# Performance work log

Hardware: AMD Instinct MI355X
Metric: run time of the kernel (lower is better)

The kernel has to match this reference:

```python
import jax, jax.numpy as jnp
import numpy as np

RADIUS = 0.1
MAX_GRID_DIM = 96
MAX_COLLISIONS = 128
INCLUDE_SELF = True


def setup_inputs() -> dict:
    key = jax.random.key(0)
    k1, k2, k3 = jax.random.split(key, 3)
    B, N, M, D, C = 2, 8192, 8192, 3, 64
    locs = jax.random.uniform(k1, (B, N, D), dtype=jnp.float32)
    data = jax.random.normal(k2, (B, N, C), dtype=jnp.float32)
    qlocs = jax.random.uniform(k3, (B, M, D), dtype=jnp.float32)
    return {"locs": locs, "data": data, "qlocs": qlocs}


def _hashgrid_order(locs):
    """Returns idxs [B,N] int32 sorting particles by flattened hash-grid cell id.
       idxs[b,i] = original index of the particle at new position i."""
    lower = jnp.min(locs, axis=1, keepdims=True)          # [B,1,D]
    upper = jnp.max(locs, axis=1, keepdims=True)          # [B,1,D]
    # grid dims per batch/dim, cell width = radius, capped at max_grid_dim
    gd = jnp.clip(jnp.floor((upper - lower) / RADIUS).astype(jnp.int32) + 1,
                  1, MAX_GRID_DIM)                        # [B,1,D]
    cell = jnp.floor((locs - lower) / RADIUS).astype(jnp.int32)
    cell = jnp.clip(cell, 0, gd - 1)                      # [B,N,D]
    # mixed-radix flatten: stride[d] = prod(gd[d+1:])
    strides = jnp.concatenate(
        [jnp.cumprod(gd[..., ::-1], axis=-1)[..., ::-1][..., 1:],
         jnp.ones_like(gd[..., :1])], axis=-1)            # [B,1,D]
    cid = jnp.sum(cell * strides, axis=-1)                # [B,N]
    return jnp.argsort(cid, axis=1, stable=True).astype(jnp.int32)


def _collisions(qlocs, nlocs):
    """For each query, indices into reordered locs within RADIUS, lowest-index
       first, padded with -1 up to MAX_COLLISIONS. Returns [B,M,K] int32."""
    B, N, _ = nlocs.shape
    d2 = jnp.sum((qlocs[:, :, None, :] - nlocs[:, None, :, :]) ** 2, axis=-1)  # [B,M,N]
    mask = d2 <= RADIUS * RADIUS
    if not INCLUDE_SELF:
        mask = mask & (d2 > 0)
    # key = particle index if neighbor else N (sentinel); first K after sort
    key = jnp.where(mask, jnp.arange(N, dtype=jnp.int32)[None, None, :], N)
    first_k = jnp.sort(key, axis=-1)[..., :MAX_COLLISIONS]                     # [B,M,K]
    return jnp.where(first_k < N, first_k, -1).astype(jnp.int32)


def reference(locs, data, qlocs):
    idxs = _hashgrid_order(locs)                              # [B,N]
    nlocs = jnp.take_along_axis(locs, idxs[..., None], axis=1)   # reordered locs
    ndata = jnp.take_along_axis(data, idxs[..., None], axis=1)   # reordered data
    neighbors = _collisions(qlocs, nlocs)                     # [B,M,K]
    return nlocs, ndata, idxs, neighbors
```

## Files before the change

kernel.cpp:

```cpp
#include <hip/hip_runtime.h>
#include <cfloat>
#include <math.h>

#define BB 2
#define NN 8192
#define MM 8192
#define CC 64
#define RAD 0.1f
#define R2 0.01f
#define MAXK 128
#define CELL_CAP 4096
#define CS_STRIDE 4100

#define WS_HDR 0
#define WS_SIDX 32
#define WS_CS (WS_SIDX + BB*NN)
#define WS_NL4 (WS_CS + BB*CS_STRIDE)

__device__ __forceinline__ int cell_of(float v, float lo, int g) {
    int c = (int)floorf(__fdiv_rn(v - lo, RAD));
    return min(max(c, 0), g - 1);
}

__global__ __launch_bounds__(1024) void build_kernel(const float* __restrict__ locs,
                                                     int* __restrict__ ws,
                                                     float* __restrict__ idxs_out) {
    const int b = blockIdx.x;
    const int t = threadIdx.x;
    const int lane = t & 63;
    const int wid = t >> 6;
    __shared__ int s_start[CELL_CAP + 1];
    __shared__ int s_aux[16];
    __shared__ int s_tmp[NN];
    __shared__ int s_cid[NN];
    __shared__ float s_red6[16 * 6];
    __shared__ float s_lo[3];
    __shared__ int   s_g[3];
    __shared__ int   s_str[2];

    const float* L = locs + (size_t)b * NN * 3;

    float mn0 = FLT_MAX, mn1 = FLT_MAX, mn2 = FLT_MAX;
    float mx0 = -FLT_MAX, mx1 = -FLT_MAX, mx2 = -FLT_MAX;
    for (int i = t; i < NN; i += 1024) {
        float x = L[i*3+0], y = L[i*3+1], z = L[i*3+2];
        mn0 = fminf(mn0, x); mx0 = fmaxf(mx0, x);
        mn1 = fminf(mn1, y); mx1 = fmaxf(mx1, y);
        mn2 = fminf(mn2, z); mx2 = fmaxf(mx2, z);
    }
    #pragma unroll
    for (int d = 1; d < 64; d <<= 1) {
        mn0 = fminf(mn0, __shfl_xor(mn0, d, 64));
        mn1 = fminf(mn1, __shfl_xor(mn1, d, 64));
        mn2 = fminf(mn2, __shfl_xor(mn2, d, 64));
        mx0 = fmaxf(mx0, __shfl_xor(mx0, d, 64));
        mx1 = fmaxf(mx1, __shfl_xor(mx1, d, 64));
        mx2 = fmaxf(mx2, __shfl_xor(mx2, d, 64));
    }
    if (lane == 0) {
        s_red6[wid*6+0] = mn0; s_red6[wid*6+1] = mn1; s_red6[wid*6+2] = mn2;
        s_red6[wid*6+3] = mx0; s_red6[wid*6+4] = mx1; s_red6[wid*6+5] = mx2;
    }
    for (int c = t; c < CELL_CAP + 1; c += 1024) s_start[c] = 0;
    __syncthreads();
    if (t == 0) {
        float lo0 = FLT_MAX, lo1 = FLT_MAX, lo2 = FLT_MAX;
        float up0 = -FLT_MAX, up1 = -FLT_MAX, up2 = -FLT_MAX;
        for (int w = 0; w < 16; ++w) {
            lo0 = fminf(lo0, s_red6[w*6+0]); lo1 = fminf(lo1, s_red6[w*6+1]);
            lo2 = fminf(lo2, s_red6[w*6+2]);
            up0 = fmaxf(up0, s_red6[w*6+3]); up1 = fmaxf(up1, s_red6[w*6+4]);
            up2 = fmaxf(up2, s_red6[w*6+5]);
        }
        int g0 = min(max((int)floorf(__fdiv_rn(up0 - lo0, RAD)) + 1, 1), 96);
        int g1 = min(max((int)floorf(__fdiv_rn(up1 - lo1, RAD)) + 1, 1), 96);
        int g2 = min(max((int)floorf(__fdiv_rn(up2 - lo2, RAD)) + 1, 1), 96);
        s_lo[0] = lo0; s_lo[1] = lo1; s_lo[2] = lo2;
        s_g[0] = g0; s_g[1] = g1; s_g[2] = g2;
        s_str[0] = g1 * g2; s_str[1] = g2;
        int* hdr = ws + WS_HDR + b * 16;
        hdr[0] = __float_as_int(lo0); hdr[1] = __float_as_int(lo1); hdr[2] = __float_as_int(lo2);
        hdr[3] = g0; hdr[4] = g1; hdr[5] = g2;
        hdr[6] = g1 * g2; hdr[7] = g2; hdr[8] = g0 * g1 * g2;
    }
    __syncthreads();
    const float lo0 = s_lo[0], lo1 = s_lo[1], lo2f = s_lo[2];
    const int g0 = s_g[0], g1 = s_g[1], g2 = s_g[2];
    const int st0 = s_str[0], st1 = s_str[1];
    const int ncells = g0 * g1 * g2;

    for (int i = t; i < NN; i += 1024) {
        int c0 = cell_of(L[i*3+0], lo0, g0);
        int c1 = cell_of(L[i*3+1], lo1, g1);
        int c2 = cell_of(L[i*3+2], lo2f, g2);
        int cid = c0*st0 + c1*st1 + c2;
        s_cid[i] = cid;
        atomicAdd(&s_start[cid], 1);
    }
    __syncthreads();

    int base4 = t * 4;
    int v0 = s_start[base4], v1 = s_start[base4+1], v2 = s_start[base4+2], v3 = s_start[base4+3];
    int sum = v0 + v1 + v2 + v3;
    int x = sum;
    #pragma unroll
    for (int d = 1; d < 64; d <<= 1) {
        int v = __shfl_up(x, d, 64);
        if (lane >= d) x += v;
    }
    if (lane == 63) s_aux[wid] = x;
    __syncthreads();
    if (wid == 0) {
        int w = (lane < 16) ? s_aux[lane] : 0;
        #pragma unroll
        for (int d = 1; d < 16; d <<= 1) {
            int v = __shfl_up(w, d, 64);
            if (lane >= d) w += v;
        }
        if (lane < 16) s_aux[lane] = w;
    }
    __syncthreads();
    int waveoff = (wid == 0) ? 0 : s_aux[wid - 1];
    int run = waveoff + x - sum;
    s_start[base4]   = run;
    s_start[base4+1] = run + v0;
    s_start[base4+2] = run + v0 + v1;
    s_start[base4+3] = run + v0 + v1 + v2;
    if (t == 1023) s_start[CELL_CAP] = run + sum;
    __syncthreads();

    for (int i = t; i < NN; i += 1024) {
        int pos = atomicAdd(&s_start[s_cid[i]], 1);
        s_tmp[pos] = i;
    }
    __syncthreads();

    int* cs = ws + WS_CS + b * CS_STRIDE;
    for (int c = t; c <= ncells; c += 1024) cs[c] = (c == 0) ? 0 : s_start[c - 1];

    int* sIdx = ws + WS_SIDX + b * NN;
    for (int p = t; p < NN; p += 1024) {
        int i = s_tmp[p];
        int cid = s_cid[i];
        int segs = (cid == 0) ? 0 : s_start[cid - 1];
        int sege = s_start[cid];
        int rank = 0;
        for (int q = segs; q < sege; ++q) rank += (s_tmp[q] < i) ? 1 : 0;
        int f = segs + rank;
        sIdx[f] = i;
        idxs_out[b * NN + f] = (float)i;
    }
}

__global__ __launch_bounds__(256) void reorder_kernel(const float* __restrict__ locs,
                                                      const float* __restrict__ data,
                                                      const int* __restrict__ ws,
                                                      float* __restrict__ nlocs_out,
                                                      float* __restrict__ ndata_out,
                                                      float* __restrict__ nlocs4) {
    int tid = blockIdx.x * 256 + threadIdx.x;
    int b = tid >> 19;
    int r = tid & ((NN * CC) - 1);
    int p = r >> 6;
    int c = r & 63;
    int idx = ws[WS_SIDX + b * NN + p];
    ndata_out[tid] = data[((size_t)b * NN + idx) * CC + c];
    if (c < 3) {
        float v = locs[((size_t)b * NN + idx) * 3 + c];
        nlocs_out[((size_t)b * NN + p) * 3 + c] = v;
        nlocs4[((size_t)b * NN + p) * 4 + c] = v;
    } else if (c == 3) {
        nlocs4[((size_t)b * NN + p) * 4 + 3] = 0.0f;
    }
}

__global__ __launch_bounds__(256) void neigh_kernel(const float* __restrict__ qlocs,
                                                    const float4* __restrict__ P4,
                                                    const int* __restrict__ ws,
                                                    float* __restrict__ neigh_out) {
    const int tid  = blockIdx.x * 256 + threadIdx.x;
    const int q    = tid >> 4;
    const int lane = threadIdx.x & 63;
    const int sub  = lane >> 4;
    const int lg   = lane & 15;
    const int b    = q >> 13;

    const int* hdr = ws + WS_HDR + b * 16;
    float lo0 = __int_as_float(hdr[0]);
    float lo1 = __int_as_float(hdr[1]);
    float lo2f = __int_as_float(hdr[2]);
    int g0 = hdr[3], g1 = hdr[4], g2 = hdr[5];
    int st0 = hdr[6], st1 = hdr[7];
    const int* cs = ws + WS_CS + b * CS_STRIDE;
    const float4* P = P4 + (size_t)b * NN;

    float qx = qlocs[(size_t)q * 3 + 0];
    float qy = qlocs[(size_t)q * 3 + 1];
    float qz = qlocs[(size_t)q * 3 + 2];

    int c0 = (int)floorf(__fdiv_rn(qx - lo0, RAD));
    int c1 = (int)floorf(__fdiv_rn(qy - lo1, RAD));
    int c2 = (int)floorf(__fdiv_rn(qz - lo2f, RAD));
    int a2lo = max(c2 - 1, 0), a2hi = min(c2 + 1, g2 - 1);
    bool zok = (a2lo <= a2hi);

    int rs[9], re[9];
    #pragma unroll
    for (int da0 = 0; da0 < 3; ++da0) {
        #pragma unroll
        for (int da1 = 0; da1 < 3; ++da1) {
            int k = da0 * 3 + da1;
            int a0 = c0 + da0 - 1;
            int a1 = c1 + da1 - 1;
            bool ok = zok && (a0 >= 0) && (a0 < g0) && (a1 >= 0) && (a1 < g1);
            int basec = a0 * st0 + a1 * st1;
            rs[k] = ok ? cs[basec + a2lo] : 0;
            re[k] = ok ? cs[basec + a2hi + 1] : 0;
        }
    }

    int cnt = 0;
    float* o = neigh_out + (size_t)q * MAXK;
    #pragma unroll
    for (int k = 0; k < 9; ++k) {
        int ps = rs[k], pe = re[k];
        for (int base = ps; base < pe; base += 16) {
            int p = base + lg;
            bool hit = false;
            if (p < pe) {
                float4 v = P[p];
                float dx = qx - v.x;
                float dy = qy - v.y;
                float dz = qz - v.z;
                float d2 = __fadd_rn(__fadd_rn(__fmul_rn(dx, dx), __fmul_rn(dy, dy)),
                                     __fmul_rn(dz, dz));
                hit = (d2 <= R2);
            }
            unsigned long long m = __ballot(hit);
            unsigned mb = (unsigned)((m >> (sub * 16)) & 0xFFFFull);
            if (hit) {
                int slot = cnt + __popc(mb & ((1u << lg) - 1u));
                if (slot < MAXK) o[slot] = (float)p;
            }
            cnt += __popc(mb);
        }
    }
    for (int s = cnt + lg; s < MAXK; s += 16) o[s] = -1.0f;
}

extern "C" void kernel_launch(void* const* d_in, const int* in_sizes, int n_in,
                              void* d_out, int out_size, void* d_ws, size_t ws_size,
                              hipStream_t stream) {
    (void)in_sizes; (void)n_in; (void)out_size; (void)ws_size;
    const float* locs  = (const float*)d_in[0];
    const float* data  = (const float*)d_in[1];
    const float* qlocs = (const float*)d_in[2];
    float* out = (float*)d_out;
    float* nlocs_out = out;
    float* ndata_out = out + BB * NN * 3;
    float* idxs_out  = out + BB * NN * 3 + BB * NN * CC;
    float* neigh_out = idxs_out + BB * NN;
    int* wsi = (int*)d_ws;
    float* nlocs4 = (float*)(wsi + WS_NL4);

    build_kernel<<<BB, 1024, 0, stream>>>(locs, wsi, idxs_out);
    reorder_kernel<<<(BB * NN * CC) / 256, 256, 0, stream>>>(locs, data, wsi,
                                                             nlocs_out, ndata_out, nlocs4);
    neigh_kernel<<<(BB * MM * 16) / 256, 256, 0, stream>>>(qlocs, (const float4*)nlocs4, wsi, neigh_out);
}
```

Measured before the change: 94.41 us.

## Use full wavefront per query, vectorize data reorder, fuse loc reorder into build

The neighbor kernel now gives each query a whole 64-lane wavefront instead of a 16-lane group. The nine cell ranges are loaded by lanes 0-8 and broadcast with shuffles, and a full 64-bit ballot drives compaction. The data reorder copies float4 vectors instead of scalars, and the sorted locations are written from the build kernel instead of the reorder kernel. Wider per-query parallelism may leave lanes idle on small cells, and the single-block build kernel takes on extra serial writes.

```diff
diff --git a/kernel.cpp b/kernel.cpp
--- a/kernel.cpp
+++ b/kernel.cpp
@@ -24,7 +24,9 @@
 
 __global__ __launch_bounds__(1024) void build_kernel(const float* __restrict__ locs,
                                                      int* __restrict__ ws,
-                                                     float* __restrict__ idxs_out) {
+                                                     float* __restrict__ idxs_out,
+                                                     float* __restrict__ nlocs_out,
+                                                     float* __restrict__ nlocs4) {
     const int b = blockIdx.x;
     const int t = threadIdx.x;
     const int lane = t & 63;
@@ -149,40 +151,32 @@
         int f = segs + rank;
         sIdx[f] = i;
         idxs_out[b * NN + f] = (float)i;
-    }
-}
-
-__global__ __launch_bounds__(256) void reorder_kernel(const float* __restrict__ locs,
-                                                      const float* __restrict__ data,
+        float x = L[i*3+0], y = L[i*3+1], z = L[i*3+2];
+        size_t o3 = ((size_t)b * NN + f) * 3;
+        nlocs_out[o3+0] = x; nlocs_out[o3+1] = y; nlocs_out[o3+2] = z;
+        float4* n4 = (float4*)nlocs4;
+        n4[(size_t)b * NN + f] = make_float4(x, y, z, 0.0f);
+    }
+}
+
+__global__ __launch_bounds__(256) void reorder_kernel(const float4* __restrict__ data4,
                                                       const int* __restrict__ ws,
-                                                      float* __restrict__ nlocs_out,
-                                                      float* __restrict__ ndata_out,
-                                                      float* __restrict__ nlocs4) {
+                                                      float4* __restrict__ ndata4) {
     int tid = blockIdx.x * 256 + threadIdx.x;
-    int b = tid >> 19;
-    int r = tid & ((NN * CC) - 1);
-    int p = r >> 6;
-    int c = r & 63;
+    int b = tid >> 17;
+    int r = tid & ((NN * 16) - 1);
+    int p = r >> 4;
+    int c4 = r & 15;
     int idx = ws[WS_SIDX + b * NN + p];
-    ndata_out[tid] = data[((size_t)b * NN + idx) * CC + c];
-    if (c < 3) {
-        float v = locs[((size_t)b * NN + idx) * 3 + c];
-        nlocs_out[((size_t)b * NN + p) * 3 + c] = v;
-        nlocs4[((size_t)b * NN + p) * 4 + c] = v;
-    } else if (c == 3) {
-        nlocs4[((size_t)b * NN + p) * 4 + 3] = 0.0f;
-    }
+    ndata4[tid] = data4[(((size_t)b * NN + idx) << 4) + c4];
 }
 
 __global__ __launch_bounds__(256) void neigh_kernel(const float* __restrict__ qlocs,
                                                     const float4* __restrict__ P4,
                                                     const int* __restrict__ ws,
                                                     float* __restrict__ neigh_out) {
-    const int tid  = blockIdx.x * 256 + threadIdx.x;
-    const int q    = tid >> 4;
+    const int q    = blockIdx.x * 4 + (threadIdx.x >> 6);
     const int lane = threadIdx.x & 63;
-    const int sub  = lane >> 4;
-    const int lg   = lane & 15;
     const int b    = q >> 13;
 
     const int* hdr = ws + WS_HDR + b * 16;
@@ -204,28 +198,24 @@
     int a2lo = max(c2 - 1, 0), a2hi = min(c2 + 1, g2 - 1);
     bool zok = (a2lo <= a2hi);
 
-    int rs[9], re[9];
-    #pragma unroll
-    for (int da0 = 0; da0 < 3; ++da0) {
-        #pragma unroll
-        for (int da1 = 0; da1 < 3; ++da1) {
-            int k = da0 * 3 + da1;
-            int a0 = c0 + da0 - 1;
-            int a1 = c1 + da1 - 1;
-            bool ok = zok && (a0 >= 0) && (a0 < g0) && (a1 >= 0) && (a1 < g1);
-            int basec = a0 * st0 + a1 * st1;
-            rs[k] = ok ? cs[basec + a2lo] : 0;
-            re[k] = ok ? cs[basec + a2hi + 1] : 0;
-        }
+    int psv = 0, pev = 0;
+    if (lane < 9) {
+        int a0 = c0 + (lane / 3) - 1;
+        int a1 = c1 + (lane % 3) - 1;
+        bool ok = zok && (a0 >= 0) && (a0 < g0) && (a1 >= 0) && (a1 < g1);
+        int basec = a0 * st0 + a1 * st1;
+        psv = ok ? cs[basec + a2lo] : 0;
+        pev = ok ? cs[basec + a2hi + 1] : 0;
     }
 
     int cnt = 0;
     float* o = neigh_out + (size_t)q * MAXK;
     #pragma unroll
     for (int k = 0; k < 9; ++k) {
-        int ps = rs[k], pe = re[k];
-        for (int base = ps; base < pe; base += 16) {
-            int p = base + lg;
+        int ps = __shfl(psv, k, 64);
+        int pe = __shfl(pev, k, 64);
+        for (int base = ps; base < pe; base += 64) {
+            int p = base + lane;
             bool hit = false;
             if (p < pe) {
                 float4 v = P[p];
@@ -237,15 +227,14 @@
                 hit = (d2 <= R2);
             }
             unsigned long long m = __ballot(hit);
-            unsigned mb = (unsigned)((m >> (sub * 16)) & 0xFFFFull);
             if (hit) {
-                int slot = cnt + __popc(mb & ((1u << lg) - 1u));
+                int slot = cnt + (int)__popcll(m & ((1ull << lane) - 1ull));
                 if (slot < MAXK) o[slot] = (float)p;
             }
-            cnt += __popc(mb);
+            cnt += (int)__popcll(m);
         }
     }
-    for (int s = cnt + lg; s < MAXK; s += 16) o[s] = -1.0f;
+    for (int s = cnt + lane; s < MAXK; s += 64) o[s] = -1.0f;
 }
 
 extern "C" void kernel_launch(void* const* d_in, const int* in_sizes, int n_in,
@@ -263,8 +252,8 @@
     int* wsi = (int*)d_ws;
     float* nlocs4 = (float*)(wsi + WS_NL4);
 
-    build_kernel<<<BB, 1024, 0, stream>>>(locs, wsi, idxs_out);
-    reorder_kernel<<<(BB * NN * CC) / 256, 256, 0, stream>>>(locs, data, wsi,
-                                                             nlocs_out, ndata_out, nlocs4);
-    neigh_kernel<<<(BB * MM * 16) / 256, 256, 0, stream>>>(qlocs, (const float4*)nlocs4, wsi, neigh_out);
-}
+    build_kernel<<<BB, 1024, 0, stream>>>(locs, wsi, idxs_out, nlocs_out, nlocs4);
+    reorder_kernel<<<(BB * NN * 16) / 256, 256, 0, stream>>>((const float4*)data, wsi,
+                                                             (float4*)ndata_out);
+    neigh_kernel<<<(BB * MM) / 4, 256, 0, stream>>>(qlocs, (const float4*)nlocs4, wsi, neigh_out);
+}
```

Result: slower. 99.81 us (+5.7%).
